# Kernel optimization log

Hardware: AMD Instinct MI355X
Metric: run time of the kernel (lower is better)

Reference implementation:

```python
import jax, jax.numpy as jnp
import numpy as np

NUM_PARTS = 2
SAMPLE_STEP = 3  # models sample_points(pts, 3, True) as deterministic stride-3 subsampling


def quat_to_rot(q):
    # wxyz quaternion -> 3x3 rotation (same formula as the torch module)
    q = q / jnp.linalg.norm(q)
    a, b, c, d = q[0], q[1], q[2], q[3]
    return jnp.stack([
        1 - 2 * c * c - 2 * d * d, 2 * b * c - 2 * a * d, 2 * a * c + 2 * b * d,
        2 * b * c + 2 * a * d, 1 - 2 * b * b - 2 * d * d, 2 * c * d - 2 * a * b,
        2 * b * d - 2 * a * c, 2 * a * b + 2 * c * d, 1 - 2 * b * b - 2 * c * c,
    ]).reshape(3, 3)


def make_transform(q, t):
    rot = quat_to_rot(q)                      # (3,3)
    top = jnp.concatenate([rot, t], axis=1)   # (3,4)
    bottom = jnp.array([[0.0, 0.0, 0.0, 1.0]], dtype=top.dtype)
    return jnp.concatenate([top, bottom], axis=0)  # (4,4)


def chamfer(x, y):
    # x: (M,4), y: (M,4) homogeneous points; symmetric chamfer of Euclidean cdist
    d2 = jnp.sum(x * x, -1)[:, None] + jnp.sum(y * y, -1)[None, :] - 2.0 * (x @ y.T)
    d = jnp.sqrt(jnp.maximum(d2, 0.0))
    return jnp.mean(jnp.min(d, axis=1)) + jnp.mean(jnp.min(d, axis=0))


def setup_inputs() -> dict:
    key = jax.random.key(0)
    ks = jax.random.split(key, 6)
    N = 24576
    camera_pts = jax.random.normal(ks[0], (NUM_PARTS, N, 3), dtype=jnp.float32)
    cad_pts = jax.random.normal(ks[1], (NUM_PARTS, N, 3), dtype=jnp.float32)
    part_weight = jax.random.uniform(ks[2], (NUM_PARTS + 1,), dtype=jnp.float32)
    rot_quat = jax.random.normal(ks[3], (NUM_PARTS, 4), dtype=jnp.float32)
    tra = jax.random.normal(ks[4], (NUM_PARTS, 3, 1), dtype=jnp.float32)
    joint_axes = jax.random.normal(ks[5], (NUM_PARTS, 2, 4), dtype=jnp.float32)
    return {"camera_pts": camera_pts, "cad_pts": cad_pts, "part_weight": part_weight,
            "rot_quat": rot_quat, "tra": tra, "joint_axes": joint_axes}


def reference(camera_pts, cad_pts, part_weight, rot_quat, tra, joint_axes):
    # stride-3 subsample, then homogenize with a ones column
    scad = cad_pts[:, ::SAMPLE_STEP]      # (P, M, 3)
    scam = camera_pts[:, ::SAMPLE_STEP]   # (P, M, 3)
    ones = jnp.ones(scad.shape[:-1] + (1,), dtype=scad.dtype)
    scad_h = jnp.concatenate([scad, ones], axis=-1)  # (P, M, 4)
    scam_h = jnp.concatenate([scam, ones], axis=-1)  # (P, M, 4)

    transforms = jax.vmap(make_transform)(rot_quat, tra)        # (P, 4, 4)
    cad_base = jnp.einsum('pij,pnj->pni', transforms, scad_h)   # (P, M, 4)

    e_geo_parts = jax.vmap(chamfer)(cad_base, scam_h)           # (P,)
    e_geo = jnp.dot(part_weight[:NUM_PARTS], e_geo_parts)

    diff = transforms[0] @ joint_axes[0].T - transforms[1] @ joint_axes[1].T  # (4, K)
    e_kin = jax.nn.sigmoid(-5.0 * jnp.linalg.norm(diff))

    all_objective = e_geo + part_weight[NUM_PARTS] * e_kin
    return all_objective, e_kin, jax.lax.stop_gradient(transforms)
```

## Files before the change

### kernel.cpp

```cpp
#include <hip/hip_runtime.h>
#include <math.h>

#define NS 8192
#define NPTS 24576
#define YSPLIT 16
#define YTILE 512
#define BX 256
#define XPT 4
#define XB (NS / (BX * XPT))

#define PARTIAL_OFF 131136

__device__ __forceinline__ void make_T12(const float* __restrict__ rq,
                                         const float* __restrict__ tra,
                                         int p, float* T) {
    float a = rq[p * 4 + 0], b = rq[p * 4 + 1];
    float c = rq[p * 4 + 2], d = rq[p * 4 + 3];
    float inv = rsqrtf(a * a + b * b + c * c + d * d);
    a *= inv; b *= inv; c *= inv; d *= inv;
    T[0]  = 1.f - 2.f * c * c - 2.f * d * d;
    T[1]  = 2.f * b * c - 2.f * a * d;
    T[2]  = 2.f * a * c + 2.f * b * d;
    T[3]  = tra[p * 3 + 0];
    T[4]  = 2.f * b * c + 2.f * a * d;
    T[5]  = 1.f - 2.f * b * b - 2.f * d * d;
    T[6]  = 2.f * c * d - 2.f * a * b;
    T[7]  = tra[p * 3 + 1];
    T[8]  = 2.f * b * d - 2.f * a * c;
    T[9]  = 2.f * a * b + 2.f * c * d;
    T[10] = 1.f - 2.f * b * b - 2.f * c * c;
    T[11] = tra[p * 3 + 2];
}

__global__ __launch_bounds__(BX) void chamfer_fused(
    const float* __restrict__ cam, const float* __restrict__ cad,
    const float* __restrict__ rq,  const float* __restrict__ tr,
    const float* __restrict__ ja,
    float* __restrict__ ws, float* __restrict__ out)
{
    int combo = blockIdx.y;
    int p   = combo >> 1;
    int dir = combo & 1;

    float T[12];
    make_T12(rq, tr, p, T);

    if (blockIdx.x == 0 && blockIdx.y == 0 && blockIdx.z == 0 && threadIdx.x == 0) {
        float TT[2][16];
        for (int q = 0; q < 2; ++q) {
            make_T12(rq, tr, q, TT[q]);
            TT[q][12] = 0.f; TT[q][13] = 0.f; TT[q][14] = 0.f; TT[q][15] = 1.f;
            for (int k = 0; k < 16; ++k) out[2 + q * 16 + k] = TT[q][k];
        }
        float ss = 0.f;
        for (int i = 0; i < 4; ++i) {
            for (int j = 0; j < 2; ++j) {
                float d0 = 0.f, d1 = 0.f;
                for (int k = 0; k < 4; ++k) {
                    d0 += TT[0][i * 4 + k] * ja[0 * 8 + j * 4 + k];
                    d1 += TT[1][i * 4 + k] * ja[1 * 8 + j * 4 + k];
                }
                float df = d0 - d1;
                ss += df * df;
            }
        }
        float ek = 1.f / (1.f + expf(5.f * sqrtf(ss)));
        ws[36] = ek;
        out[1] = ek;
        ws[0] = 0.f; ws[1] = 0.f; ws[2] = 0.f; ws[3] = 0.f;
        *(int*)(ws + 40) = 0;
    }

    int xbase = blockIdx.x * (BX * XPT) + threadIdx.x;
    const float* xsrc = (dir == 0 ? cad : cam) + p * NPTS * 3;
    float m0[XPT], m1[XPT], m2[XPT], s[XPT], dmin[XPT];
#pragma unroll
    for (int k = 0; k < XPT; ++k) {
        int i = xbase + k * BX;
        const float* sp = xsrc + i * 9;
        float x = sp[0], y = sp[1], z = sp[2];
        if (dir == 0) {
            float tx = T[0] * x + T[1] * y + T[2]  * z + T[3];
            float ty = T[4] * x + T[5] * y + T[6]  * z + T[7];
            float tz = T[8] * x + T[9] * y + T[10] * z + T[11];
            x = tx; y = ty; z = tz;
        }
        m0[k] = -2.f * x; m1[k] = -2.f * y; m2[k] = -2.f * z;
        s[k]  = x * x + y * y + z * z;
        dmin[k] = 3.4e38f;
    }

    __shared__ float4 sy[YTILE];
    const float* ysrc = (dir == 0 ? cam : cad) + p * NPTS * 3;
    int ybase = blockIdx.z * YTILE;
#pragma unroll
    for (int t = 0; t < YTILE / BX; ++t) {
        int i = ybase + t * BX + threadIdx.x;
        const float* sp = ysrc + i * 9;
        float x = sp[0], y = sp[1], z = sp[2];
        if (dir == 1) {
            float tx = T[0] * x + T[1] * y + T[2]  * z + T[3];
            float ty = T[4] * x + T[5] * y + T[6]  * z + T[7];
            float tz = T[8] * x + T[9] * y + T[10] * z + T[11];
            x = tx; y = ty; z = tz;
        }
        sy[t * BX + threadIdx.x] = make_float4(x, y, z, x * x + y * y + z * z);
    }
    __syncthreads();

#pragma unroll 4
    for (int j = 0; j < YTILE; j += 2) {
        float4 ya = sy[j];
        float4 yb = sy[j + 1];
#pragma unroll
        for (int k = 0; k < XPT; ++k) {
            float da = fmaf(m0[k], ya.x, ya.w);
            da = fmaf(m1[k], ya.y, da);
            da = fmaf(m2[k], ya.z, da);
            float db = fmaf(m0[k], yb.x, yb.w);
            db = fmaf(m1[k], yb.y, db);
            db = fmaf(m2[k], yb.z, db);
            dmin[k] = fminf(dmin[k], fminf(da, db));
        }
    }

    float* partial = ws + PARTIAL_OFF + combo * (YSPLIT * NS) + blockIdx.z * NS;
#pragma unroll
    for (int k = 0; k < XPT; ++k) {
        partial[xbase + k * BX] = s[k] + dmin[k];
    }
}

__global__ __launch_bounds__(256) void reduce_final(
    float* __restrict__ ws, const float* __restrict__ pw,
    float* __restrict__ out)
{
    int combo = blockIdx.y;
    int x = blockIdx.x * 256 + threadIdx.x;
    const float* p = ws + PARTIAL_OFF + combo * (YSPLIT * NS) + x;
    float m = p[0];
#pragma unroll
    for (int ysi = 1; ysi < YSPLIT; ++ysi) m = fminf(m, p[ysi * NS]);
    float d = sqrtf(fmaxf(m, 0.f));
#pragma unroll
    for (int off = 32; off > 0; off >>= 1) d += __shfl_down(d, off, 64);

    __shared__ float sm[4];
    __shared__ bool last;
    int wid = threadIdx.x >> 6;
    if ((threadIdx.x & 63) == 0) sm[wid] = d;
    __syncthreads();
    if (threadIdx.x == 0) {
        float sum = sm[0] + sm[1] + sm[2] + sm[3];
        atomicAdd(&ws[combo], sum);
        __threadfence();
        int t = atomicAdd((int*)(ws + 40), 1);
        last = (t == 4 * (NS / 256) - 1);
    }
    __syncthreads();
    if (last && threadIdx.x == 0) {
        float a0 = atomicAdd(&ws[0], 0.f);
        float a1 = atomicAdd(&ws[1], 0.f);
        float a2 = atomicAdd(&ws[2], 0.f);
        float a3 = atomicAdd(&ws[3], 0.f);
        float e0 = (a0 + a1) * (1.f / NS);
        float e1 = (a2 + a3) * (1.f / NS);
        out[0] = pw[0] * e0 + pw[1] * e1 + pw[2] * ws[36];
    }
}

extern "C" void kernel_launch(void* const* d_in, const int* in_sizes, int n_in,
                              void* d_out, int out_size, void* d_ws, size_t ws_size,
                              hipStream_t stream) {
    const float* cam = (const float*)d_in[0];
    const float* cad = (const float*)d_in[1];
    const float* pw  = (const float*)d_in[2];
    const float* rq  = (const float*)d_in[3];
    const float* tr  = (const float*)d_in[4];
    const float* ja  = (const float*)d_in[5];
    float* out = (float*)d_out;
    float* ws  = (float*)d_ws;

    dim3 cg(XB, 4, YSPLIT);
    chamfer_fused<<<cg, BX, 0, stream>>>(cam, cad, rq, tr, ja, ws, out);
    reduce_final<<<dim3(NS / 256, 4), 256, 0, stream>>>(ws, pw, out);
}
```

Measured before the change: 94.21 us.

## Fuse final reduction into chamfer kernel via per-slab last-block atomics

Removes the separate reduce kernel. Each chamfer block increments a per-slab counter, and the last of the YSPLIT blocks for that slab does the min-over-splits and sqrt-sum. A global counter then picks the final block, which computes the kinematic term and the objective. The workspace counters are zeroed with a memset before the launch. This saves a kernel launch and the dependency gap between kernels, at the cost of extra atomics and a memset node.

```diff
diff --git a/kernel.cpp b/kernel.cpp
--- a/kernel.cpp
+++ b/kernel.cpp
@@ -8,6 +8,7 @@
 #define BX 256
 #define XPT 4
 #define XB (NS / (BX * XPT))
+#define NSLAB (4 * XB)
 
 #define PARTIAL_OFF 131136
 
@@ -32,10 +33,10 @@
     T[11] = tra[p * 3 + 2];
 }
 
-__global__ __launch_bounds__(BX) void chamfer_fused(
+__global__ __launch_bounds__(BX) void chamfer_all(
     const float* __restrict__ cam, const float* __restrict__ cad,
     const float* __restrict__ rq,  const float* __restrict__ tr,
-    const float* __restrict__ ja,
+    const float* __restrict__ ja,  const float* __restrict__ pw,
     float* __restrict__ ws, float* __restrict__ out)
 {
     int combo = blockIdx.y;
@@ -44,32 +45,6 @@
 
     float T[12];
     make_T12(rq, tr, p, T);
-
-    if (blockIdx.x == 0 && blockIdx.y == 0 && blockIdx.z == 0 && threadIdx.x == 0) {
-        float TT[2][16];
-        for (int q = 0; q < 2; ++q) {
-            make_T12(rq, tr, q, TT[q]);
-            TT[q][12] = 0.f; TT[q][13] = 0.f; TT[q][14] = 0.f; TT[q][15] = 1.f;
-            for (int k = 0; k < 16; ++k) out[2 + q * 16 + k] = TT[q][k];
-        }
-        float ss = 0.f;
-        for (int i = 0; i < 4; ++i) {
-            for (int j = 0; j < 2; ++j) {
-                float d0 = 0.f, d1 = 0.f;
-                for (int k = 0; k < 4; ++k) {
-                    d0 += TT[0][i * 4 + k] * ja[0 * 8 + j * 4 + k];
-                    d1 += TT[1][i * 4 + k] * ja[1 * 8 + j * 4 + k];
-                }
-                float df = d0 - d1;
-                ss += df * df;
-            }
-        }
-        float ek = 1.f / (1.f + expf(5.f * sqrtf(ss)));
-        ws[36] = ek;
-        out[1] = ek;
-        ws[0] = 0.f; ws[1] = 0.f; ws[2] = 0.f; ws[3] = 0.f;
-        *(int*)(ws + 40) = 0;
-    }
 
     int xbase = blockIdx.x * (BX * XPT) + threadIdx.x;
     const float* xsrc = (dir == 0 ? cad : cam) + p * NPTS * 3;
@@ -129,44 +104,71 @@
     for (int k = 0; k < XPT; ++k) {
         partial[xbase + k * BX] = s[k] + dmin[k];
     }
-}
 
-__global__ __launch_bounds__(256) void reduce_final(
-    float* __restrict__ ws, const float* __restrict__ pw,
-    float* __restrict__ out)
-{
-    int combo = blockIdx.y;
-    int x = blockIdx.x * 256 + threadIdx.x;
-    const float* p = ws + PARTIAL_OFF + combo * (YSPLIT * NS) + x;
-    float m = p[0];
-#pragma unroll
-    for (int ysi = 1; ysi < YSPLIT; ++ysi) m = fminf(m, p[ysi * NS]);
-    float d = sqrtf(fmaxf(m, 0.f));
-#pragma unroll
-    for (int off = 32; off > 0; off >>= 1) d += __shfl_down(d, off, 64);
-
-    __shared__ float sm[4];
-    __shared__ bool last;
-    int wid = threadIdx.x >> 6;
-    if ((threadIdx.x & 63) == 0) sm[wid] = d;
-    __syncthreads();
+    __threadfence();
+    __shared__ int lastflag;
+    int slab = combo * XB + blockIdx.x;
     if (threadIdx.x == 0) {
-        float sum = sm[0] + sm[1] + sm[2] + sm[3];
-        atomicAdd(&ws[combo], sum);
-        __threadfence();
-        int t = atomicAdd((int*)(ws + 40), 1);
-        last = (t == 4 * (NS / 256) - 1);
+        int t = atomicAdd((int*)ws + 8 + slab, 1);
+        lastflag = (t == YSPLIT - 1);
     }
     __syncthreads();
-    if (last && threadIdx.x == 0) {
-        float a0 = atomicAdd(&ws[0], 0.f);
-        float a1 = atomicAdd(&ws[1], 0.f);
-        float a2 = atomicAdd(&ws[2], 0.f);
-        float a3 = atomicAdd(&ws[3], 0.f);
-        float e0 = (a0 + a1) * (1.f / NS);
-        float e1 = (a2 + a3) * (1.f / NS);
-        out[0] = pw[0] * e0 + pw[1] * e1 + pw[2] * ws[36];
+    if (!lastflag) return;
+
+    const float* pbase = ws + PARTIAL_OFF + combo * (YSPLIT * NS) + blockIdx.x * (BX * XPT);
+    float dsum = 0.f;
+#pragma unroll
+    for (int k = 0; k < XPT; ++k) {
+        int x = k * BX + threadIdx.x;
+        float m = pbase[x];
+#pragma unroll
+        for (int z = 1; z < YSPLIT; ++z) m = fminf(m, pbase[z * NS + x]);
+        dsum += sqrtf(fmaxf(m, 0.f));
     }
+#pragma unroll
+    for (int off = 32; off > 0; off >>= 1) dsum += __shfl_down(dsum, off, 64);
+
+    __shared__ float sm[BX / 64];
+    int wid = threadIdx.x >> 6;
+    if ((threadIdx.x & 63) == 0) sm[wid] = dsum;
+    __syncthreads();
+    if (threadIdx.x != 0) return;
+
+    float bs = sm[0] + sm[1] + sm[2] + sm[3];
+    atomicAdd(&ws[combo], bs);
+    __threadfence();
+    int g = atomicAdd((int*)ws + 4, 1);
+    if (g != NSLAB - 1) return;
+
+    float a0 = atomicAdd(&ws[0], 0.f);
+    float a1 = atomicAdd(&ws[1], 0.f);
+    float a2 = atomicAdd(&ws[2], 0.f);
+    float a3 = atomicAdd(&ws[3], 0.f);
+
+    float TT[2][16];
+    for (int q = 0; q < 2; ++q) {
+        make_T12(rq, tr, q, TT[q]);
+        TT[q][12] = 0.f; TT[q][13] = 0.f; TT[q][14] = 0.f; TT[q][15] = 1.f;
+        for (int k = 0; k < 16; ++k) out[2 + q * 16 + k] = TT[q][k];
+    }
+    float ss = 0.f;
+    for (int i = 0; i < 4; ++i) {
+        for (int j = 0; j < 2; ++j) {
+            float d0 = 0.f, d1 = 0.f;
+            for (int k = 0; k < 4; ++k) {
+                d0 += TT[0][i * 4 + k] * ja[0 * 8 + j * 4 + k];
+                d1 += TT[1][i * 4 + k] * ja[1 * 8 + j * 4 + k];
+            }
+            float df = d0 - d1;
+            ss += df * df;
+        }
+    }
+    float ek = 1.f / (1.f + expf(5.f * sqrtf(ss)));
+    out[1] = ek;
+
+    float e0 = (a0 + a1) * (1.f / NS);
+    float e1 = (a2 + a3) * (1.f / NS);
+    out[0] = pw[0] * e0 + pw[1] * e1 + pw[2] * ek;
 }
 
 extern "C" void kernel_launch(void* const* d_in, const int* in_sizes, int n_in,
@@ -181,7 +183,8 @@
     float* out = (float*)d_out;
     float* ws  = (float*)d_ws;
 
+    hipMemsetAsync(ws, 0, 160, stream);
+
     dim3 cg(XB, 4, YSPLIT);
-    chamfer_fused<<<cg, BX, 0, stream>>>(cam, cad, rq, tr, ja, ws, out);
-    reduce_final<<<dim3(NS / 256, 4), 256, 0, stream>>>(ws, pw, out);
+    chamfer_all<<<cg, BX, 0, stream>>>(cam, cad, rq, tr, ja, pw, ws, out);
 }
```

Result: slower. 134.2 us (+42.4%).

## Split Y range finer and parallelize reduction over Y splits

Applied to the files above, without the earlier changes.

Raises the number of Y splits from 16 to 64 with smaller Y tiles, which gives the chamfer kernel four times as many blocks and more parallelism across the GPU. The reduction kernel is restructured so each block covers 64 x-points, with four wavefronts each taking a quarter of the Y splits before combining through shared memory. The cost is four times the partial-min traffic written to and read from the workspace, more per-block setup, and a larger grid of atomics in the reduction. Unused rotation and translation pointers are added to the reduction kernel's arguments.

```diff
diff --git a/kernel.cpp b/kernel.cpp
--- a/kernel.cpp
+++ b/kernel.cpp
@@ -3,13 +3,14 @@
 
 #define NS 8192
 #define NPTS 24576
-#define YSPLIT 16
-#define YTILE 512
+#define YSPLIT 64
+#define YTILE 128
 #define BX 256
 #define XPT 4
 #define XB (NS / (BX * XPT))
 
 #define PARTIAL_OFF 131136
+#define RED_BLOCKS (4 * (NS / 64))
 
 __device__ __forceinline__ void make_T12(const float* __restrict__ rq,
                                          const float* __restrict__ tra,
@@ -93,10 +94,8 @@
     __shared__ float4 sy[YTILE];
     const float* ysrc = (dir == 0 ? cam : cad) + p * NPTS * 3;
     int ybase = blockIdx.z * YTILE;
-#pragma unroll
-    for (int t = 0; t < YTILE / BX; ++t) {
-        int i = ybase + t * BX + threadIdx.x;
-        const float* sp = ysrc + i * 9;
+    for (int t = threadIdx.x; t < YTILE; t += BX) {
+        const float* sp = ysrc + (ybase + t) * 9;
         float x = sp[0], y = sp[1], z = sp[2];
         if (dir == 1) {
             float tx = T[0] * x + T[1] * y + T[2]  * z + T[3];
@@ -104,7 +103,7 @@
             float tz = T[8] * x + T[9] * y + T[10] * z + T[11];
             x = tx; y = ty; z = tz;
         }
-        sy[t * BX + threadIdx.x] = make_float4(x, y, z, x * x + y * y + z * z);
+        sy[t] = make_float4(x, y, z, x * x + y * y + z * z);
     }
     __syncthreads();
 
@@ -133,40 +132,43 @@
 
 __global__ __launch_bounds__(256) void reduce_final(
     float* __restrict__ ws, const float* __restrict__ pw,
+    const float* __restrict__ rq, const float* __restrict__ tr,
     float* __restrict__ out)
 {
     int combo = blockIdx.y;
-    int x = blockIdx.x * 256 + threadIdx.x;
-    const float* p = ws + PARTIAL_OFF + combo * (YSPLIT * NS) + x;
-    float m = p[0];
+    int lane = threadIdx.x & 63;
+    int zg   = threadIdx.x >> 6;
+    const float* p = ws + PARTIAL_OFF + combo * (YSPLIT * NS)
+                   + blockIdx.x * 64 + lane;
+    float m = 3.4e38f;
 #pragma unroll
-    for (int ysi = 1; ysi < YSPLIT; ++ysi) m = fminf(m, p[ysi * NS]);
-    float d = sqrtf(fmaxf(m, 0.f));
+    for (int z = 0; z < YSPLIT / 4; ++z)
+        m = fminf(m, p[(zg * (YSPLIT / 4) + z) * NS]);
+
+    __shared__ float sm[4][64];
+    sm[zg][lane] = m;
+    __syncthreads();
+    if (zg != 0) return;
+
+    float mm = fminf(fminf(sm[0][lane], sm[1][lane]),
+                     fminf(sm[2][lane], sm[3][lane]));
+    float d = sqrtf(fmaxf(mm, 0.f));
 #pragma unroll
     for (int off = 32; off > 0; off >>= 1) d += __shfl_down(d, off, 64);
+    if (lane != 0) return;
 
-    __shared__ float sm[4];
-    __shared__ bool last;
-    int wid = threadIdx.x >> 6;
-    if ((threadIdx.x & 63) == 0) sm[wid] = d;
-    __syncthreads();
-    if (threadIdx.x == 0) {
-        float sum = sm[0] + sm[1] + sm[2] + sm[3];
-        atomicAdd(&ws[combo], sum);
-        __threadfence();
-        int t = atomicAdd((int*)(ws + 40), 1);
-        last = (t == 4 * (NS / 256) - 1);
-    }
-    __syncthreads();
-    if (last && threadIdx.x == 0) {
-        float a0 = atomicAdd(&ws[0], 0.f);
-        float a1 = atomicAdd(&ws[1], 0.f);
-        float a2 = atomicAdd(&ws[2], 0.f);
-        float a3 = atomicAdd(&ws[3], 0.f);
-        float e0 = (a0 + a1) * (1.f / NS);
-        float e1 = (a2 + a3) * (1.f / NS);
-        out[0] = pw[0] * e0 + pw[1] * e1 + pw[2] * ws[36];
-    }
+    atomicAdd(&ws[combo], d);
+    __threadfence();
+    int t = atomicAdd((int*)(ws + 40), 1);
+    if (t != RED_BLOCKS - 1) return;
+
+    float a0 = atomicAdd(&ws[0], 0.f);
+    float a1 = atomicAdd(&ws[1], 0.f);
+    float a2 = atomicAdd(&ws[2], 0.f);
+    float a3 = atomicAdd(&ws[3], 0.f);
+    float e0 = (a0 + a1) * (1.f / NS);
+    float e1 = (a2 + a3) * (1.f / NS);
+    out[0] = pw[0] * e0 + pw[1] * e1 + pw[2] * ws[36];
 }
 
 extern "C" void kernel_launch(void* const* d_in, const int* in_sizes, int n_in,
@@ -183,5 +185,5 @@
 
     dim3 cg(XB, 4, YSPLIT);
     chamfer_fused<<<cg, BX, 0, stream>>>(cam, cad, rq, tr, ja, ws, out);
-    reduce_final<<<dim3(NS / 256, 4), 256, 0, stream>>>(ws, pw, out);
+    reduce_final<<<dim3(NS / 64, 4), 256, 0, stream>>>(ws, pw, rq, tr, out);
 }
```

After: 104.8 us. 11.2% more time.
